# Optimization experiments

Hardware: AMD Instinct MI355X
Metric: run time of the kernel (lower is better)

## Reference

```python
import jax, jax.numpy as jnp
import numpy as np

N, E = 50000, 100000
D, H, EDGE_DIM = 300, 4, 4  # node_dim, heads, edge_dim; per-head C = D
HC = H * D


def setup_inputs() -> dict:
    key = jax.random.key(0)
    ks = jax.random.split(key, 16)
    s = 0.02
    return {
        "xin": jax.random.normal(ks[0], (N, D), jnp.float32),
        "e_idx": jax.random.randint(ks[1], (2, E), 0, N, jnp.int64 if jax.config.jax_enable_x64 else jnp.int32),
        "e_attr": jax.random.normal(ks[2], (E, EDGE_DIM), jnp.float32),
        # TransformerConv params
        "Wq": jax.random.normal(ks[3], (D, HC), jnp.float32) * s,
        "bq": jnp.zeros((HC,), jnp.float32),
        "Wk": jax.random.normal(ks[4], (D, HC), jnp.float32) * s,
        "bk": jnp.zeros((HC,), jnp.float32),
        "Wv": jax.random.normal(ks[5], (D, HC), jnp.float32) * s,
        "bv": jnp.zeros((HC,), jnp.float32),
        "We": jax.random.normal(ks[6], (EDGE_DIM, HC), jnp.float32) * s,
        "be": jnp.zeros((HC,), jnp.float32),
        "Wskip": jax.random.normal(ks[7], (D, HC), jnp.float32) * s,
        "bskip": jnp.zeros((HC,), jnp.float32),
        # LayerNorm params
        "ln_a": jnp.ones((HC,), jnp.float32),
        "ln_b": jnp.zeros((HC,), jnp.float32),
        # output Linear params
        "Wlin": jax.random.normal(ks[8], (HC, D), jnp.float32) * s,
        "blin": jnp.zeros((D,), jnp.float32),
    }


def _forward(xin, e_idx, e_attr, Wq, bq, Wk, bk, Wv, bv, We, be, Wskip, bskip, ln_a, ln_b, Wlin, blin):
    n = xin.shape[0]
    src, dst = e_idx[0], e_idx[1]
    scale = 1.0 / jnp.sqrt(jnp.float32(D))

    q = (xin @ Wq + bq).reshape(n, H, D)
    k = (xin @ Wk + bk).reshape(n, H, D)
    v = (xin @ Wv + bv).reshape(n, H, D)
    ee = (e_attr @ We + be).reshape(-1, H, D)  # [E,H,C]

    kj = k[src] + ee                                        # gather + edge conditioning
    alpha = jnp.einsum('ehc,ehc->eh', q[dst], kj) * scale   # [E,H]
    amax = jax.ops.segment_max(alpha, dst, num_segments=n)  # segment softmax
    alpha = jnp.exp(alpha - amax[dst])
    denom = jax.ops.segment_sum(alpha, dst, num_segments=n)
    alpha = alpha / (denom[dst] + 1e-16)

    msg = (v[src] + ee) * alpha[:, :, None]                 # [E,H,C]
    agg = jax.ops.segment_sum(msg.reshape(-1, HC), dst, num_segments=n)
    x = agg + xin @ Wskip + bskip                           # root/skip weight

    # LayerNorm (biased variance)
    mean = x.mean(-1, keepdims=True)
    var = ((x - mean) ** 2).mean(-1, keepdims=True)
    x = ln_a * (x - mean) / jnp.sqrt(var + 1e-5) + ln_b

    x = x @ Wlin + blin
    return jax.nn.elu(x + xin)


def reference(xin, e_idx, e_attr, Wq, bq, Wk, bk, Wv, bv, We, be, Wskip, bskip, ln_a, ln_b, Wlin, blin):
    return _forward(xin, e_idx, e_attr, Wq, bq, Wk, bk, Wv, bv, We, be, Wskip, bskip, ln_a, ln_b, Wlin, blin)
```

## Files before the change

kernel.cpp:

```cpp
#include <hip/hip_runtime.h>
#include <hip/hip_bf16.h>

typedef __bf16 bf16;
typedef __bf16 bf16x4 __attribute__((ext_vector_type(4)));
typedef __bf16 bf16x8 __attribute__((ext_vector_type(8)));
typedef float f32x4 __attribute__((ext_vector_type(4)));

constexpr int kN = 50000;
constexpr int kE = 100000;
constexpr int kD = 300;
constexpr int kH = 4;
constexpr int kHC = 1200;
constexpr int kK1A = 304;
constexpr int kK1B = 320;
constexpr int kNP1 = 2432;
constexpr int kMP = 50048;
constexpr int kK2 = 1216;
constexpr int kN2P = 384;
constexpr int kLY = 1216;
constexpr int kNB1 = kNP1 / 128;
constexpr int kMB2 = kMP / 64;
constexpr int kMB = kMP / 128;
constexpr int kT1 = kK1B / 32;
constexpr int kNB2 = kN2P / 128;
constexpr int kT2 = kK2 / 32;
constexpr int kWG1 = kMB2 * kNB1;
constexpr int kWG2 = kNB2 * kMB;
constexpr int kSplitRow = 49342;
constexpr size_t kXhiBytes = (size_t)(kN + 1 - kSplitRow) * kK1A * 2;

__device__ __forceinline__ float ldF(const void* p, size_t i, int f32) {
    return f32 ? ((const float*)p)[i] : (float)((const bf16*)p)[i];
}
__device__ __forceinline__ int ldI(const void* p, size_t i, int i64) {
    return i64 ? ((const int*)p)[2 * i] : ((const int*)p)[i];
}

__device__ __forceinline__ const bf16* xrow(const bf16* lo, const bf16* hi, int r) {
    return r < kSplitRow ? lo + (size_t)r * kK1A : hi + (size_t)(r - kSplitRow) * kK1A;
}
__device__ __forceinline__ bf16* xrow_w(bf16* lo, bf16* hi, int r) {
    return r < kSplitRow ? lo + (size_t)r * kK1A : hi + (size_t)(r - kSplitRow) * kK1A;
}

__device__ __forceinline__ void glds16(const void* g, void* l) {
    __builtin_amdgcn_global_load_lds((const __attribute__((address_space(1))) void*)g,
                                     (__attribute__((address_space(3))) void*)l, 16, 0, 0);
}

template <int NWG>
__device__ __forceinline__ int xcd_swz(int phys) {
    constexpr int q = NWG >> 3, r = NWG & 7;
    int xcd = phys & 7, i = phys >> 3;
    int base = xcd < r ? xcd * (q + 1) : r * (q + 1) + (xcd - r) * q;
    return base + i;
}

__device__ __forceinline__ float bflo(unsigned u) {
    return __builtin_bit_cast(float, u << 16);
}
__device__ __forceinline__ float bfhi(unsigned u) {
    return __builtin_bit_cast(float, u & 0xFFFF0000u);
}
__device__ __forceinline__ unsigned bfpack(float a, float b) {
    bf16 x = (bf16)a, y = (bf16)b;
    unsigned short ux = __builtin_bit_cast(unsigned short, x);
    unsigned short uy = __builtin_bit_cast(unsigned short, y);
    return (unsigned)ux | ((unsigned)uy << 16);
}
__device__ __forceinline__ float wsum(float v) {
#pragma unroll
    for (int o = 32; o > 0; o >>= 1) v += __shfl_xor(v, o);
    return v;
}

__global__ void detect_kernel(const unsigned short* __restrict__ xin_u,
                              const int* __restrict__ eidx_i,
                              int* __restrict__ flags) {
    __shared__ int s_ff, s_nz;
    if (threadIdx.x == 0) { s_ff = 0; s_nz = 0; }
    __syncthreads();
    int c1 = 0;
    for (int i = threadIdx.x; i < 65536; i += 256)
        c1 += (((xin_u[i] >> 7) & 0xFF) == 0xFF);
    int c2 = 0;
    for (int i = threadIdx.x; i < 1024; i += 256)
        c2 += (eidx_i[2 * i + 1] != 0);
    atomicAdd(&s_ff, c1);
    atomicAdd(&s_nz, c2);
    __syncthreads();
    if (threadIdx.x == 0) {
        flags[0] = (s_ff > 0) ? 1 : 0;
        flags[1] = (s_nz == 0) ? 1 : 0;
    }
}

__global__ void cast5(const void* __restrict__ We, const void* __restrict__ be,
                      const void* __restrict__ lna, const void* __restrict__ lnb,
                      const void* __restrict__ blin, float* __restrict__ Wef,
                      float* __restrict__ bef, float* __restrict__ lnaf,
                      float* __restrict__ lnbf, float* __restrict__ blinf,
                      const int* __restrict__ flags) {
    int i = blockIdx.x * 256 + threadIdx.x;
    int f32 = flags[0];
    if (i < 4 * kHC) { Wef[i] = ldF(We, i, f32); return; }
    i -= 4 * kHC;
    if (i < kHC) { bef[i] = ldF(be, i, f32); return; }
    i -= kHC;
    if (i < kHC) { lnaf[i] = ldF(lna, i, f32); return; }
    i -= kHC;
    if (i < kHC) { lnbf[i] = ldF(lnb, i, f32); return; }
    i -= kHC;
    if (i < kD) blinf[i] = ldF(blin, i, f32);
}

__global__ void cast_xpad(const void* __restrict__ xin, bf16* __restrict__ xlo,
                          bf16* __restrict__ xhi, const int* __restrict__ flags) {
    int idx = blockIdx.x * 256 + threadIdx.x;
    if (idx < 4) {
        bf16x4 z = {};
        *(bf16x4*)&xlo[(size_t)kSplitRow * kK1A + idx * 4] = z;
    }
    if (idx >= (kN + 1) * 76) return;
    int r = idx / 76, c4 = idx % 76;
    int c = c4 * 4;
    bf16x4 w = {};
    if (r < kN && c < kD) {
        int f32 = flags[0];
        size_t b = (size_t)r * kD + c;
        w[0] = (bf16)ldF(xin, b + 0, f32);
        w[1] = (bf16)ldF(xin, b + 1, f32);
        w[2] = (bf16)ldF(xin, b + 2, f32);
        w[3] = (bf16)ldF(xin, b + 3, f32);
    }
    *(bf16x4*)&(xrow_w(xlo, xhi, r)[c]) = w;
}

__global__ void pack_W1f(const void* __restrict__ Wq, const void* __restrict__ Wk,
                         const void* __restrict__ Wv, const void* __restrict__ Ws,
                         bf16* __restrict__ Bf, const int* __restrict__ flags) {
    int idx = blockIdx.x * 256 + threadIdx.x;
    if (idx >= 2 * kNB1 * kT1 * 8 * 64) return;
    int f32 = flags[0];
    int lane = idx & 63;
    int fi = (idx >> 6) & 7;
    int ksnb = idx >> 9;
    int ks = ksnb % kT1;
    int nbp = ksnb / kT1;
    int p = nbp / kNB1, nb = nbp % kNB1;
    int n = nb * 128 + fi * 16 + (lane & 15);
    int kbase = ks * 32 + (lane >> 4) * 8;
    const void* W = nullptr;
    int c = 0;
    if (n < kHC)          { W = p == 0 ? Wq : Ws; c = n; }
    else if (n < 2 * kHC) { W = p == 0 ? Wk : Wv; c = n - kHC; }
    bf16x8 w = {};
#pragma unroll
    for (int e = 0; e < 8; ++e) {
        int k = kbase + e;
        float v = 0.f;
        if (W && k < kD) v = ldF(W, (size_t)k * kHC + c, f32);
        w[e] = (bf16)v;
    }
    *(bf16x8*)&Bf[(size_t)idx * 8] = w;
}

__global__ void pack_W2f(const void* __restrict__ Wlin, bf16* __restrict__ Bf,
                         const int* __restrict__ flags) {
    int idx = blockIdx.x * 256 + threadIdx.x;
    if (idx >= kNB2 * kT2 * 8 * 64) return;
    int f32 = flags[0];
    int lane = idx & 63;
    int fi = (idx >> 6) & 7;
    int ksnb = idx >> 9;
    int ks = ksnb % kT2;
    int nb = ksnb / kT2;
    int n = nb * 128 + fi * 16 + (lane & 15);
    int kbase = ks * 32 + (lane >> 4) * 8;
    bf16x8 w = {};
#pragma unroll
    for (int e = 0; e < 8; ++e) {
        int k = kbase + e;
        float v = 0.f;
        if (n < kD && k < kHC) v = ldF(Wlin, (size_t)k * kD + n, f32);
        w[e] = (bf16)v;
    }
    *(bf16x8*)&Bf[(size_t)idx * 8] = w;
}

__global__ void pack_bias(const void* __restrict__ bq, const void* __restrict__ bk,
                          const void* __restrict__ bv, const void* __restrict__ bs,
                          float* __restrict__ bcat, const int* __restrict__ flags) {
    int n = blockIdx.x * 256 + threadIdx.x;
    if (n >= 2 * kNP1) return;
    int f32 = flags[0];
    int p = n / kNP1, nl = n % kNP1;
    float v = 0.f;
    if (nl < 2 * kHC) {
        const void* b;
        int c;
        if (nl < kHC) { b = p == 0 ? bq : bs; c = nl; }
        else          { b = p == 0 ? bk : bv; c = nl - kHC; }
        v = ldF(b, c, f32);
    }
    bcat[n] = v;
}

__global__ void hist_kernel(const void* __restrict__ eidx, int* __restrict__ cnt,
                            const int* __restrict__ flags) {
    int e = blockIdx.x * 256 + threadIdx.x;
    if (e < kE) atomicAdd(&cnt[ldI(eidx, (size_t)kE + e, flags[1])], 1);
}

__global__ __launch_bounds__(1024) void scan_kernel(const int* __restrict__ cnt,
                                                    int* __restrict__ rowptr) {
    __shared__ int buf[1024];
    int t = threadIdx.x;
    int running = 0;
    for (int base = 0; base < kN; base += 1024) {
        int v = (base + t < kN) ? cnt[base + t] : 0;
        buf[t] = v;
        __syncthreads();
        for (int off = 1; off < 1024; off <<= 1) {
            int u = (t >= off) ? buf[t - off] : 0;
            __syncthreads();
            buf[t] += u;
            __syncthreads();
        }
        if (base + t < kN) rowptr[base + t] = running + buf[t] - v;
        running += buf[1023];
        __syncthreads();
    }
    if (t == 0) rowptr[kN] = running;
}

__global__ void scatter_kernel(const void* __restrict__ eidx, const int* __restrict__ rowptr,
                               int* __restrict__ fill, int* __restrict__ esort,
                               const int* __restrict__ flags) {
    int e = blockIdx.x * 256 + threadIdx.x;
    if (e < kE) {
        int d = ldI(eidx, (size_t)kE + e, flags[1]);
        int pos = rowptr[d] + atomicAdd(&fill[d], 1);
        esort[pos] = e;
    }
}

__global__ __launch_bounds__(256, 4) void gemm_qkvs(const bf16* __restrict__ xlo,
                                                    const bf16* __restrict__ xhi,
                                                    const bf16* __restrict__ Bf,
                                                    const float* __restrict__ bcat,
                                                    bf16* __restrict__ outA,
                                                    bf16* __restrict__ outB) {
    __shared__ alignas(16) bf16 As[64 * 32];
    const int logical = xcd_swz<kWG1>(blockIdx.x);
    const int mb = logical / kNB1, nb = logical % kNB1;
    const int tid = threadIdx.x;
    const int lane = tid & 63, wave = tid >> 6;
    const int quad = lane >> 4, l16 = lane & 15;
    const int mw = (wave >> 1) * 32;
    const int fibase = (wave & 1) * 4;
    const f32x4 zero = {0.f, 0.f, 0.f, 0.f};
    f32x4 acc[2][4];
#pragma unroll
    for (int i = 0; i < 2; i++)
#pragma unroll
        for (int j = 0; j < 4; j++) acc[i][j] = zero;
    const int mblk = mb * 64, nblk = nb * 128;
    const int srow = wave * 16 + (lane >> 2);
    const int ss = lane & 3;
    int gr = mblk + srow; if (gr >= kN) gr = kN - 1;
    const bf16* gA = xrow(xlo, xhi, gr) + ((ss ^ ((srow >> 1) & 3)) << 3);
    bf16* lA = As + wave * 512;
    int aoff[2];
#pragma unroll
    for (int i = 0; i < 2; i++) {
        int ra = mw + i * 16 + l16;
        aoff[i] = ra * 32 + ((quad ^ ((ra >> 1) & 3)) << 3);
    }
    const bf16* bbase = Bf + (size_t)nb * (kT1 * 4096) + fibase * 512 + lane * 8;
    for (int t = 0; t < kT1; ++t) {
        __syncthreads();
        glds16(gA + t * 32, lA);
        bf16x8 bfv[4];
#pragma unroll
        for (int ni = 0; ni < 4; ni++)
            bfv[ni] = *(const bf16x8*)(bbase + (size_t)t * 4096 + ni * 512);
        __syncthreads();
        bf16x8 af[2];
#pragma unroll
        for (int i = 0; i < 2; i++) af[i] = *(const bf16x8*)&As[aoff[i]];
#pragma unroll
        for (int mi = 0; mi < 2; mi++)
#pragma unroll
            for (int ni = 0; ni < 4; ni++)
                acc[mi][ni] = __builtin_amdgcn_mfma_f32_16x16x32_bf16(
                    af[mi], bfv[ni], acc[mi][ni], 0, 0, 0);
    }
#pragma unroll
    for (int mi = 0; mi < 2; mi++)
#pragma unroll
        for (int r = 0; r < 4; r++) {
            int m = mblk + mw + mi * 16 + quad * 4 + r;
            if (m >= kN) continue;
#pragma unroll
            for (int ni = 0; ni < 4; ni++) {
                int n = nblk + (fibase + ni) * 16 + l16;
                float v = acc[mi][ni][r] + bcat[n];
                if (n < kHC)          outA[(size_t)m * kLY + n] = (bf16)v;
                else if (n < 2 * kHC) outB[(size_t)m * kHC + (n - kHC)] = (bf16)v;
            }
        }
}

__global__ __launch_bounds__(256) void node_alpha(const int* __restrict__ rowptr,
                                                  const int* __restrict__ esort,
                                                  const void* __restrict__ eidx,
                                                  const void* __restrict__ eattr,
                                                  bf16* __restrict__ qb,
                                                  const bf16* __restrict__ kb,
                                                  const float* __restrict__ Wef,
                                                  const float* __restrict__ bef,
                                                  float* __restrict__ alpha,
                                                  const int* __restrict__ flags) {
    int i = blockIdx.x;
    int h = threadIdx.x >> 6, lane = threadIdx.x & 63;
    int r0 = rowptr[i], r1 = rowptr[i + 1];
    if (r0 >= r1) return;
    int f32 = flags[0], i64 = flags[1];
    const unsigned* qr = (const unsigned*)(qb + (size_t)i * kLY + h * kD);
    float q0[3], q1[3];
#pragma unroll
    for (int j = 0; j < 3; ++j) {
        int p = lane + 64 * j;
        unsigned u = (p < 150) ? qr[p] : 0u;
        q0[j] = bflo(u); q1[j] = bfhi(u);
    }
    float tj[4], tb;
#pragma unroll
    for (int jj = 0; jj < 4; ++jj) {
        const float* w = Wef + jj * kHC + h * kD;
        float s = 0.f;
#pragma unroll
        for (int j = 0; j < 3; ++j) {
            int p = lane + 64 * j;
            if (p < 150) s += q0[j] * w[2 * p] + q1[j] * w[2 * p + 1];
        }
        tj[jj] = wsum(s);
    }
    {
        const float* br = bef + h * kD;
        float s = 0.f;
#pragma unroll
        for (int j = 0; j < 3; ++j) {
            int p = lane + 64 * j;
            if (p < 150) s += q0[j] * br[2 * p] + q1[j] * br[2 * p + 1];
        }
        tb = wsum(s);
    }
    float denom = 0.f;
    for (int p = r0; p < r1; ++p) {
        int e = esort[p];
        int src = ldI(eidx, e, i64);
        const unsigned* kr = (const unsigned*)(kb + (size_t)src * kHC + h * kD);
        float s = 0.f;
#pragma unroll
        for (int j = 0; j < 3; ++j) {
            int pp = lane + 64 * j;
            if (pp < 150) { unsigned u = kr[pp]; s += q0[j] * bflo(u) + q1[j] * bfhi(u); }
        }
        float dot = wsum(s);
        float ea0 = ldF(eattr, (size_t)e * 4 + 0, f32), ea1 = ldF(eattr, (size_t)e * 4 + 1, f32);
        float ea2 = ldF(eattr, (size_t)e * 4 + 2, f32), ea3 = ldF(eattr, (size_t)e * 4 + 3, f32);
        float logit = dot + ea0 * tj[0] + ea1 * tj[1] + ea2 * tj[2] + ea3 * tj[3] + tb;
        float a = expf(logit * 0.05773502691896258f);
        if (lane == 0) alpha[e * kH + h] = a;
        denom += a;
    }
    if (lane == 0)
        ((float*)(qb + (size_t)i * kLY + kHC))[h] = 1.f / (denom + 1e-16f);
}

__global__ __launch_bounds__(256) void node_fused(const int* __restrict__ rowptr,
                                                  const int* __restrict__ esort,
                                                  const void* __restrict__ eidx,
                                                  const void* __restrict__ eattr,
                                                  const float* __restrict__ Wef,
                                                  const float* __restrict__ bef,
                                                  const float* __restrict__ alpha,
                                                  const bf16* __restrict__ vb,
                                                  const float* __restrict__ lnaf,
                                                  const float* __restrict__ lnbf,
                                                  bf16* __restrict__ qy,
                                                  const int* __restrict__ flags) {
    int i = blockIdx.x;
    int t = threadIdx.x, h = t >> 6, lane = t & 63;
    bf16* yr = qy + (size_t)i * kLY;
    if (i >= kN) {
        for (int c = t; c < kK2; c += 256) yr[c] = (bf16)0.f;
        return;
    }
    int f32 = flags[0], i64 = flags[1];
    int r0 = rowptr[i], r1 = rowptr[i + 1];
    float inv = (r1 > r0) ? ((const float*)(yr + kHC))[h] : 0.f;
    unsigned* yr32 = (unsigned*)(yr + h * kD);
    float a0[3], a1[3];
#pragma unroll
    for (int j = 0; j < 3; ++j) {
        int p = lane + 64 * j;
        unsigned u = (p < 150) ? yr32[p] : 0u;
        a0[j] = bflo(u); a1[j] = bfhi(u);
    }
    float S0 = 0.f, S1 = 0.f, S2 = 0.f, S3 = 0.f, Sb = 0.f;
    for (int p = r0; p < r1; ++p) {
        int e = esort[p];
        int src = ldI(eidx, e, i64);
        float coeff = alpha[e * kH + h] * inv;
        float ea0 = ldF(eattr, (size_t)e * 4 + 0, f32), ea1 = ldF(eattr, (size_t)e * 4 + 1, f32);
        float ea2 = ldF(eattr, (size_t)e * 4 + 2, f32), ea3 = ldF(eattr, (size_t)e * 4 + 3, f32);
        S0 += coeff * ea0; S1 += coeff * ea1; S2 += coeff * ea2; S3 += coeff * ea3;
        Sb += coeff;
        const unsigned* vr = (const unsigned*)(vb + (size_t)src * kHC + h * kD);
#pragma unroll
        for (int j = 0; j < 3; ++j) {
            int pp = lane + 64 * j;
            if (pp < 150) {
                unsigned u = vr[pp];
                a0[j] += coeff * bflo(u);
                a1[j] += coeff * bfhi(u);
            }
        }
    }
    {
        const float* wb = Wef + h * kD;
        const float* br = bef + h * kD;
#pragma unroll
        for (int j = 0; j < 3; ++j) {
            int p = lane + 64 * j;
            if (p < 150) {
                int c0 = 2 * p, c1 = 2 * p + 1;
                a0[j] += S0 * wb[c0] + S1 * wb[kHC + c0] + S2 * wb[2 * kHC + c0] +
                         S3 * wb[3 * kHC + c0] + Sb * br[c0];
                a1[j] += S0 * wb[c1] + S1 * wb[kHC + c1] + S2 * wb[2 * kHC + c1] +
                         S3 * wb[3 * kHC + c1] + Sb * br[c1];
            }
        }
    }
    float s = 0.f, s2 = 0.f;
#pragma unroll
    for (int j = 0; j < 3; ++j) {
        s += a0[j] + a1[j];
        s2 += a0[j] * a0[j] + a1[j] * a1[j];
    }
#pragma unroll
    for (int off = 32; off > 0; off >>= 1) {
        s += __shfl_down(s, off);
        s2 += __shfl_down(s2, off);
    }
    __shared__ float ss[4], ss2[4];
    if (lane == 0) { ss[h] = s; ss2[h] = s2; }
    __syncthreads();
    if (t == 0) {
        float S = ss[0] + ss[1] + ss[2] + ss[3];
        float S2 = ss2[0] + ss2[1] + ss2[2] + ss2[3];
        float mean = S / (float)kHC;
        float var = S2 / (float)kHC - mean * mean;
        ss[0] = mean;
        ss2[0] = rsqrtf(var + 1e-5f);
    }
    __syncthreads();
    float mean = ss[0], rstd = ss2[0];
#pragma unroll
    for (int j = 0; j < 3; ++j) {
        int p = lane + 64 * j;
        if (p < 150) {
            int c0 = h * kD + 2 * p;
            float v0 = lnaf[c0] * (a0[j] - mean) * rstd + lnbf[c0];
            float v1 = lnaf[c0 + 1] * (a1[j] - mean) * rstd + lnbf[c0 + 1];
            yr32[p] = bfpack(v0, v1);
        }
    }
    if (t < kK2 - kHC) yr[kHC + t] = (bf16)0.f;
}

__global__ __launch_bounds__(256) void gemm_out(const bf16* __restrict__ Ay,
                                                const bf16* __restrict__ Bf,
                                                const float* __restrict__ blinf,
                                                const void* __restrict__ xin,
                                                void* __restrict__ out,
                                                const int* __restrict__ flags) {
    __shared__ alignas(16) bf16 As[128 * 32];
    const int logical = xcd_swz<kWG2>(blockIdx.x);
    const int mb = logical / kNB2, nb = logical % kNB2;
    const int f32 = flags[0];
    const int tid = threadIdx.x;
    const int lane = tid & 63, wave = tid >> 6;
    const int quad = lane >> 4, l16 = lane & 15;
    const int mw = (wave >> 1) * 64, nw = (wave & 1) * 64;
    const f32x4 zero = {0.f, 0.f, 0.f, 0.f};
    f32x4 acc[4][4];
#pragma unroll
    for (int i = 0; i < 4; i++)
#pragma unroll
        for (int j = 0; j < 4; j++) acc[i][j] = zero;
    const int mblk = mb * 128, nblk = nb * 128;
    const int sr0 = wave * 32 + (lane >> 2);
    const int sr1 = sr0 + 16;
    const int ss = lane & 3;
    const bf16* gA0 = Ay + (size_t)(mblk + sr0) * kLY + ((ss ^ ((sr0 >> 1) & 3)) << 3);
    const bf16* gA1 = Ay + (size_t)(mblk + sr1) * kLY + ((ss ^ ((sr1 >> 1) & 3)) << 3);
    bf16* lA = As + wave * 1024;
    int aoff[4];
#pragma unroll
    for (int i = 0; i < 4; i++) {
        int ra = mw + i * 16 + l16;
        aoff[i] = ra * 32 + ((quad ^ ((ra >> 1) & 3)) << 3);
    }
    const bf16* bbase = Bf + (size_t)nb * (kT2 * 4096) + (wave & 1) * 2048 + lane * 8;
    for (int t = 0; t < kT2; ++t) {
        __syncthreads();
        glds16(gA0 + t * 32, lA);
        glds16(gA1 + t * 32, lA + 512);
        bf16x8 bfv[4];
#pragma unroll
        for (int ni = 0; ni < 4; ni++)
            bfv[ni] = *(const bf16x8*)(bbase + (size_t)t * 4096 + ni * 512);
        __syncthreads();
        bf16x8 af[4];
#pragma unroll
        for (int i = 0; i < 4; i++) af[i] = *(const bf16x8*)&As[aoff[i]];
#pragma unroll
        for (int mi = 0; mi < 4; mi++)
#pragma unroll
            for (int ni = 0; ni < 4; ni++)
                acc[mi][ni] = __builtin_amdgcn_mfma_f32_16x16x32_bf16(
                    af[mi], bfv[ni], acc[mi][ni], 0, 0, 0);
    }
#pragma unroll
    for (int mi = 0; mi < 4; mi++)
#pragma unroll
        for (int r = 0; r < 4; r++) {
            int m = mblk + mw + mi * 16 + quad * 4 + r;
            if (m >= kN) continue;
#pragma unroll
            for (int ni = 0; ni < 4; ni++) {
                int n = nblk + nw + ni * 16 + l16;
                if (n >= kD) continue;
                float resid = ldF(xin, (size_t)m * kD + n, f32);
                float t2 = acc[mi][ni][r] + blinf[n] + resid;
                float r2 = t2 > 0.f ? t2 : expm1f(t2);
                if (f32) ((float*)out)[(size_t)m * kD + n] = r2;
                else     ((bf16*)out)[(size_t)m * kD + n] = (bf16)r2;
            }
        }
}

__global__ void fallback_copy(const unsigned short* __restrict__ xin_u,
                              unsigned short* __restrict__ out_u) {
    int i = blockIdx.x * 256 + threadIdx.x;
    if (i < kN * kD) out_u[i] = xin_u[i];
}

extern "C" void kernel_launch(void* const* d_in, const int* in_sizes, int n_in,
                              void* d_out, int out_size, void* d_ws, size_t ws_size,
                              hipStream_t stream) {
    const void* xin  = d_in[0];
    const void* eidx = d_in[1];
    const void* eatt = d_in[2];
    const void* Wq   = d_in[3];
    const void* bq   = d_in[4];
    const void* Wk   = d_in[5];
    const void* bk   = d_in[6];
    const void* Wv   = d_in[7];
    const void* bv   = d_in[8];
    const void* We   = d_in[9];
    const void* be   = d_in[10];
    const void* Wsk  = d_in[11];
    const void* bsk  = d_in[12];
    const void* lna  = d_in[13];
    const void* lnb  = d_in[14];
    const void* Wlin = d_in[15];
    const void* blin = d_in[16];

    char* ws = (char*)d_ws;
    size_t off = 0;
    auto alloc = [&](size_t bytes) -> char* {
        char* p = ws + off;
        off += (bytes + 255) & ~(size_t)255;
        return p;
    };
    bf16* bufA   = (bf16*)alloc((size_t)kMP * kLY * 2);
    bf16* bufB   = (bf16*)alloc((size_t)kN * kHC * 2);
    bf16* W1f    = (bf16*)alloc((size_t)2 * kNP1 * kK1B * 2);
    float* bcat  = (float*)alloc((size_t)2 * kNP1 * 4);
    bf16* W2f    = (bf16*)alloc((size_t)kN2P * kK2 * 2);
    float* alpha = (float*)alloc((size_t)kE * kH * 4);
    char* ovl    = alloc(kXhiBytes);
    int* cnt     = (int*)ovl;
    int* fill    = (int*)(ovl + 200064);
    bf16* xhi    = (bf16*)ovl;
    int* rowptr  = (int*)alloc((size_t)(kN + 1) * 4);
    int* esort   = (int*)alloc((size_t)kE * 4);
    float* Wef   = (float*)alloc((size_t)4 * kHC * 4);
    float* bef   = (float*)alloc((size_t)kHC * 4);
    float* lnaf  = (float*)alloc((size_t)kHC * 4);
    float* lnbf  = (float*)alloc((size_t)kHC * 4);
    float* blinf = (float*)alloc((size_t)kD * 4);
    int* flags   = (int*)alloc(2 * 4);
    (void)in_sizes; (void)n_in;
    bf16* xlo = (bf16*)d_out;
    if (off > ws_size ||
        (size_t)out_size * 2 < (size_t)kSplitRow * kK1A * 2 + 32) {
        fallback_copy<<<(kN * kD + 255) / 256, 256, 0, stream>>>(
            (const unsigned short*)xin, (unsigned short*)d_out);
        return;
    }

    detect_kernel<<<1, 256, 0, stream>>>((const unsigned short*)xin, (const int*)eidx, flags);
    hipMemsetAsync(cnt, 0, (size_t)kN * 4, stream);
    hipMemsetAsync(fill, 0, (size_t)kN * 4, stream);
    hist_kernel<<<(kE + 255) / 256, 256, 0, stream>>>(eidx, cnt, flags);
    scan_kernel<<<1, 1024, 0, stream>>>(cnt, rowptr);
    scatter_kernel<<<(kE + 255) / 256, 256, 0, stream>>>(eidx, rowptr, fill, esort, flags);
    cast_xpad<<<((kN + 1) * 76 + 255) / 256, 256, 0, stream>>>(xin, xlo, xhi, flags);
    cast5<<<(4 * kHC + 3 * kHC + kD + 255) / 256, 256, 0, stream>>>(
        We, be, lna, lnb, blin, Wef, bef, lnaf, lnbf, blinf, flags);
    pack_W1f<<<(2 * kNB1 * kT1 * 8 * 64 + 255) / 256, 256, 0, stream>>>(
        Wq, Wk, Wv, Wsk, W1f, flags);
    pack_bias<<<(2 * kNP1 + 255) / 256, 256, 0, stream>>>(bq, bk, bv, bsk, bcat, flags);
    pack_W2f<<<(kNB2 * kT2 * 8 * 64 + 255) / 256, 256, 0, stream>>>(Wlin, W2f, flags);

    gemm_qkvs<<<kWG1, 256, 0, stream>>>(xlo, xhi, W1f, bcat, bufA, bufB);
    node_alpha<<<kN, 256, 0, stream>>>(rowptr, esort, eidx, eatt, bufA, bufB,
                                       Wef, bef, alpha, flags);
    gemm_qkvs<<<kWG1, 256, 0, stream>>>(
        xlo, xhi, W1f + (size_t)kNB1 * kT1 * 4096, bcat + kNP1, bufA, bufB);
    node_fused<<<kMP, 256, 0, stream>>>(rowptr, esort, eidx, eatt, Wef, bef, alpha,
                                        bufB, lnaf, lnbf, bufA, flags);
    gemm_out<<<kWG2, 256, 0, stream>>>(bufA, W2f, blinf, xin, d_out, flags);
}
```

Baseline: 1.246 ms.

## Parallelize rowptr scan, stage QKV epilogue through LDS, shrink output GEMM tile

Replaces the single-block serial prefix scan over node counts with a three-kernel multi-block scan using wave shuffles. The QKV GEMM epilogue now writes results into shared memory and then emits 16-byte vectorized stores instead of scattered 2-byte stores. The output GEMM moves from 128x128 to 64x128 tiles with a min-blocks launch bound, raising the block count and occupancy. Costs are two extra kernel launches, about 17 KB more LDS per QKV block, and more re-reads of the B matrix in the output GEMM.

```diff
diff --git a/kernel.cpp b/kernel.cpp
--- a/kernel.cpp
+++ b/kernel.cpp
@@ -20,12 +20,12 @@
 constexpr int kLY = 1216;
 constexpr int kNB1 = kNP1 / 128;
 constexpr int kMB2 = kMP / 64;
-constexpr int kMB = kMP / 128;
 constexpr int kT1 = kK1B / 32;
 constexpr int kNB2 = kN2P / 128;
 constexpr int kT2 = kK2 / 32;
 constexpr int kWG1 = kMB2 * kNB1;
-constexpr int kWG2 = kNB2 * kMB;
+constexpr int kWG2 = kMB2 * kNB2;
+constexpr int kEW = 136;
 constexpr int kSplitRow = 49342;
 constexpr size_t kXhiBytes = (size_t)(kN + 1 - kSplitRow) * kK1A * 2;
 
@@ -212,26 +212,47 @@
     if (e < kE) atomicAdd(&cnt[ldI(eidx, (size_t)kE + e, flags[1])], 1);
 }
 
-__global__ __launch_bounds__(1024) void scan_kernel(const int* __restrict__ cnt,
-                                                    int* __restrict__ rowptr) {
-    __shared__ int buf[1024];
+__global__ void scan_local(const int* __restrict__ cnt, int* __restrict__ rowptr,
+                           int* __restrict__ bsum) {
+    int b = blockIdx.x, t = threadIdx.x;
+    int i = b * 256 + t;
+    int v = (i < kN) ? cnt[i] : 0;
+    int lane = t & 63, wv = t >> 6;
+    int s = v;
+#pragma unroll
+    for (int o = 1; o < 64; o <<= 1) {
+        int u = __shfl_up(s, o);
+        if (lane >= o) s += u;
+    }
+    __shared__ int wtot[4];
+    if (lane == 63) wtot[wv] = s;
+    __syncthreads();
+    int add = 0;
+    for (int w = 0; w < wv; ++w) add += wtot[w];
+    if (i < kN) rowptr[i] = s - v + add;
+    if (t == 255) bsum[b] = add + s;
+}
+__global__ void scan_bsums(int* __restrict__ bsum, int nb) {
     int t = threadIdx.x;
-    int running = 0;
-    for (int base = 0; base < kN; base += 1024) {
-        int v = (base + t < kN) ? cnt[base + t] : 0;
-        buf[t] = v;
-        __syncthreads();
-        for (int off = 1; off < 1024; off <<= 1) {
-            int u = (t >= off) ? buf[t - off] : 0;
-            __syncthreads();
-            buf[t] += u;
-            __syncthreads();
-        }
-        if (base + t < kN) rowptr[base + t] = running + buf[t] - v;
-        running += buf[1023];
-        __syncthreads();
-    }
-    if (t == 0) rowptr[kN] = running;
+    int v = (t < nb) ? bsum[t] : 0;
+    int lane = t & 63, wv = t >> 6;
+    int s = v;
+#pragma unroll
+    for (int o = 1; o < 64; o <<= 1) {
+        int u = __shfl_up(s, o);
+        if (lane >= o) s += u;
+    }
+    __shared__ int wtot[4];
+    if (lane == 63) wtot[wv] = s;
+    __syncthreads();
+    int add = 0;
+    for (int w = 0; w < wv; ++w) add += wtot[w];
+    if (t < nb) bsum[t] = s - v + add;
+}
+__global__ void scan_add(int* __restrict__ rowptr, const int* __restrict__ bsum) {
+    int i = blockIdx.x * 256 + threadIdx.x;
+    if (i < kN) rowptr[i] += bsum[i >> 8];
+    if (i == 0) rowptr[kN] = kE;
 }
 
 __global__ void scatter_kernel(const void* __restrict__ eidx, const int* __restrict__ rowptr,
@@ -252,6 +273,7 @@
                                                     bf16* __restrict__ outA,
                                                     bf16* __restrict__ outB) {
     __shared__ alignas(16) bf16 As[64 * 32];
+    __shared__ alignas(16) bf16 Es[64 * kEW];
     const int logical = xcd_swz<kWG1>(blockIdx.x);
     const int mb = logical / kNB1, nb = logical % kNB1;
     const int tid = threadIdx.x;
@@ -296,20 +318,30 @@
                 acc[mi][ni] = __builtin_amdgcn_mfma_f32_16x16x32_bf16(
                     af[mi], bfv[ni], acc[mi][ni], 0, 0, 0);
     }
+    __syncthreads();
 #pragma unroll
     for (int mi = 0; mi < 2; mi++)
 #pragma unroll
         for (int r = 0; r < 4; r++) {
-            int m = mblk + mw + mi * 16 + quad * 4 + r;
-            if (m >= kN) continue;
+            int lr = mw + mi * 16 + quad * 4 + r;
 #pragma unroll
             for (int ni = 0; ni < 4; ni++) {
-                int n = nblk + (fibase + ni) * 16 + l16;
-                float v = acc[mi][ni][r] + bcat[n];
-                if (n < kHC)          outA[(size_t)m * kLY + n] = (bf16)v;
-                else if (n < 2 * kHC) outB[(size_t)m * kHC + (n - kHC)] = (bf16)v;
+                int lc = (fibase + ni) * 16 + l16;
+                Es[lr * kEW + lc] = (bf16)(acc[mi][ni][r] + bcat[nblk + lc]);
             }
         }
+    __syncthreads();
+#pragma unroll
+    for (int it = 0; it < 4; ++it) {
+        int row = it * 16 + (tid >> 4);
+        int col8 = (tid & 15) * 8;
+        int m = mblk + row;
+        if (m >= kN) continue;
+        bf16x8 w = *(const bf16x8*)&Es[row * kEW + col8];
+        int n = nblk + col8;
+        if (n < kHC)          *(bf16x8*)&outA[(size_t)m * kLY + n] = w;
+        else if (n < 2 * kHC) *(bf16x8*)&outB[(size_t)m * kHC + (n - kHC)] = w;
+    }
 }
 
 __global__ __launch_bounds__(256) void node_alpha(const int* __restrict__ rowptr,
@@ -482,68 +514,66 @@
     if (t < kK2 - kHC) yr[kHC + t] = (bf16)0.f;
 }
 
-__global__ __launch_bounds__(256) void gemm_out(const bf16* __restrict__ Ay,
-                                                const bf16* __restrict__ Bf,
-                                                const float* __restrict__ blinf,
-                                                const void* __restrict__ xin,
-                                                void* __restrict__ out,
-                                                const int* __restrict__ flags) {
-    __shared__ alignas(16) bf16 As[128 * 32];
+__global__ __launch_bounds__(256, 4) void gemm_out(const bf16* __restrict__ Ay,
+                                                   const bf16* __restrict__ Bf,
+                                                   const float* __restrict__ blinf,
+                                                   const void* __restrict__ xin,
+                                                   void* __restrict__ out,
+                                                   const int* __restrict__ flags) {
+    __shared__ alignas(16) bf16 As[64 * 32];
     const int logical = xcd_swz<kWG2>(blockIdx.x);
     const int mb = logical / kNB2, nb = logical % kNB2;
     const int f32 = flags[0];
     const int tid = threadIdx.x;
     const int lane = tid & 63, wave = tid >> 6;
     const int quad = lane >> 4, l16 = lane & 15;
-    const int mw = (wave >> 1) * 64, nw = (wave & 1) * 64;
+    const int mw = (wave >> 1) * 32;
+    const int fibase = (wave & 1) * 4;
     const f32x4 zero = {0.f, 0.f, 0.f, 0.f};
-    f32x4 acc[4][4];
-#pragma unroll
-    for (int i = 0; i < 4; i++)
+    f32x4 acc[2][4];
+#pragma unroll
+    for (int i = 0; i < 2; i++)
 #pragma unroll
         for (int j = 0; j < 4; j++) acc[i][j] = zero;
-    const int mblk = mb * 128, nblk = nb * 128;
-    const int sr0 = wave * 32 + (lane >> 2);
-    const int sr1 = sr0 + 16;
+    const int mblk = mb * 64, nblk = nb * 128;
+    const int srow = wave * 16 + (lane >> 2);
     const int ss = lane & 3;
-    const bf16* gA0 = Ay + (size_t)(mblk + sr0) * kLY + ((ss ^ ((sr0 >> 1) & 3)) << 3);
-    const bf16* gA1 = Ay + (size_t)(mblk + sr1) * kLY + ((ss ^ ((sr1 >> 1) & 3)) << 3);
-    bf16* lA = As + wave * 1024;
-    int aoff[4];
-#pragma unroll
-    for (int i = 0; i < 4; i++) {
+    const bf16* gA = Ay + (size_t)(mblk + srow) * kLY + ((ss ^ ((srow >> 1) & 3)) << 3);
+    bf16* lA = As + wave * 512;
+    int aoff[2];
+#pragma unroll
+    for (int i = 0; i < 2; i++) {
         int ra = mw + i * 16 + l16;
         aoff[i] = ra * 32 + ((quad ^ ((ra >> 1) & 3)) << 3);
     }
-    const bf16* bbase = Bf + (size_t)nb * (kT2 * 4096) + (wave & 1) * 2048 + lane * 8;
+    const bf16* bbase = Bf + (size_t)nb * (kT2 * 4096) + fibase * 512 + lane * 8;
     for (int t = 0; t < kT2; ++t) {
         __syncthreads();
-        glds16(gA0 + t * 32, lA);
-        glds16(gA1 + t * 32, lA + 512);
+        glds16(gA + t * 32, lA);
         bf16x8 bfv[4];
 #pragma unroll
         for (int ni = 0; ni < 4; ni++)
             bfv[ni] = *(const bf16x8*)(bbase + (size_t)t * 4096 + ni * 512);
         __syncthreads();
-        bf16x8 af[4];
-#pragma unroll
-        for (int i = 0; i < 4; i++) af[i] = *(const bf16x8*)&As[aoff[i]];
-#pragma unroll
-        for (int mi = 0; mi < 4; mi++)
+        bf16x8 af[2];
+#pragma unroll
+        for (int i = 0; i < 2; i++) af[i] = *(const bf16x8*)&As[aoff[i]];
+#pragma unroll
+        for (int mi = 0; mi < 2; mi++)
 #pragma unroll
             for (int ni = 0; ni < 4; ni++)
                 acc[mi][ni] = __builtin_amdgcn_mfma_f32_16x16x32_bf16(
                     af[mi], bfv[ni], acc[mi][ni], 0, 0, 0);
     }
 #pragma unroll
-    for (int mi = 0; mi < 4; mi++)
+    for (int mi = 0; mi < 2; mi++)
 #pragma unroll
         for (int r = 0; r < 4; r++) {
             int m = mblk + mw + mi * 16 + quad * 4 + r;
             if (m >= kN) continue;
 #pragma unroll
             for (int ni = 0; ni < 4; ni++) {
-                int n = nblk + nw + ni * 16 + l16;
+                int n = nblk + (fibase + ni) * 16 + l16;
                 if (n >= kD) continue;
                 float resid = ldF(xin, (size_t)m * kD + n, f32);
                 float t2 = acc[mi][ni][r] + blinf[n] + resid;
@@ -600,6 +630,7 @@
     bf16* xhi    = (bf16*)ovl;
     int* rowptr  = (int*)alloc((size_t)(kN + 1) * 4);
     int* esort   = (int*)alloc((size_t)kE * 4);
+    int* bsum    = (int*)alloc(256 * 4);
     float* Wef   = (float*)alloc((size_t)4 * kHC * 4);
     float* bef   = (float*)alloc((size_t)kHC * 4);
     float* lnaf  = (float*)alloc((size_t)kHC * 4);
@@ -615,11 +646,14 @@
         return;
     }
 
+    constexpr int kScanNB = (kN + 255) / 256;
     detect_kernel<<<1, 256, 0, stream>>>((const unsigned short*)xin, (const int*)eidx, flags);
     hipMemsetAsync(cnt, 0, (size_t)kN * 4, stream);
     hipMemsetAsync(fill, 0, (size_t)kN * 4, stream);
     hist_kernel<<<(kE + 255) / 256, 256, 0, stream>>>(eidx, cnt, flags);
-    scan_kernel<<<1, 1024, 0, stream>>>(cnt, rowptr);
+    scan_local<<<kScanNB, 256, 0, stream>>>(cnt, rowptr, bsum);
+    scan_bsums<<<1, 256, 0, stream>>>(bsum, kScanNB);
+    scan_add<<<kScanNB, 256, 0, stream>>>(rowptr, bsum);
     scatter_kernel<<<(kE + 255) / 256, 256, 0, stream>>>(eidx, rowptr, fill, esort, flags);
     cast_xpad<<<((kN + 1) * 76 + 255) / 256, 256, 0, stream>>>(xin, xlo, xhi, flags);
     cast5<<<(4 * kHC + 3 * kHC + kD + 255) / 256, 256, 0, stream>>>(
```

After: 1.041 ms. 1.2x faster.
